# Optimization experiments

Measured on AMD Instinct MI355X. Metric: run time of the kernel, lower is better.

Reference implementation:

```python
import jax, jax.numpy as jnp
import numpy as np

B, T, C, H = 8, 2048, 1024, 64  # batch, context_length, embedding_dim, head_size


def setup_inputs() -> dict:
    key = jax.random.key(0)
    kx, kq, kk, kv = jax.random.split(key, 4)
    s = C ** -0.5  # linear-init-like scale
    return {
        "x": jax.random.normal(kx, (B, T, C), dtype=jnp.float32),
        "Wq": jax.random.normal(kq, (C, H), dtype=jnp.float32) * s,
        "Wk": jax.random.normal(kk, (C, H), dtype=jnp.float32) * s,
        "Wv": jax.random.normal(kv, (C, H), dtype=jnp.float32) * s,
    }


def reference(x, Wq, Wk, Wv):
    Bx, Tx, _ = x.shape
    q = jnp.einsum('btc,ch->bth', x, Wq)
    k = jnp.einsum('btc,ch->bth', x, Wk)
    v = jnp.einsum('btc,ch->bth', x, Wv)
    scale = k.shape[-1] ** -0.5
    scores = jnp.einsum('bth,bsh->bts', q, k) * scale  # [B, T, T]
    causal = jnp.tril(jnp.ones((Tx, Tx), dtype=bool))
    scores = jnp.where(causal, scores, -jnp.inf)
    weights = jax.nn.softmax(scores, axis=-1)
    # dropout is identity in eval mode
    out = jnp.einsum('bts,bsh->bth', weights, v)  # [B, T, H]
    return out
```

## Files before the change

### kernel.cpp

```cpp
#include <hip/hip_runtime.h>
#include <hip/hip_bf16.h>

#define BB 8
#define TT 2048
#define CC 1024
#define HH 64

typedef float f32x4 __attribute__((ext_vector_type(4)));
typedef float f32x16 __attribute__((ext_vector_type(16)));
typedef short s16x8 __attribute__((ext_vector_type(8)));

static __device__ __forceinline__ unsigned short f2bf(float f) {
    unsigned int u = __float_as_uint(f);
    u = (u + 0x7FFFu + ((u >> 16) & 1u)) >> 16;
    return (unsigned short)u;
}

static __device__ __forceinline__ unsigned cvt_pk_bf16(float lo, float hi) {
    unsigned r;
    asm("v_cvt_pk_bf16_f32 %0, %1, %2" : "=v"(r) : "v"(lo), "v"(hi));
    return r;
}

__global__ __launch_bounds__(256) void wt_kernel(
    const float* __restrict__ Wq, const float* __restrict__ Wk,
    const float* __restrict__ Wv, unsigned short* __restrict__ wTf) {
    const int e8 = blockIdx.x * 256 + threadIdx.x;
    const int lane = e8 & 63;
    const int s = (e8 >> 6) & 31;
    const int n16 = e8 >> 11;
    const int sel = n16 >> 2;
    const float* W = (sel == 0) ? Wq : ((sel == 1) ? Wk : Wv);
    const int h = ((n16 & 3) << 4) + (lane & 15);
    const int cb = s * 32 + ((lane >> 4) << 3);
    s16x8 v;
#pragma unroll
    for (int j = 0; j < 8; ++j) v[j] = (short)f2bf(W[(size_t)(cb + j) * HH + h]);
    *reinterpret_cast<s16x8*>(&wTf[(size_t)e8 * 8]) = v;
}

__global__ __launch_bounds__(512, 2) void qkv_kernel(
    const float* __restrict__ x, const unsigned short* __restrict__ wTf,
    unsigned short* __restrict__ Qf, unsigned short* __restrict__ Kf,
    unsigned short* __restrict__ Vf) {
    __shared__ unsigned short xb[2][64 * 128];
    const int tid = threadIdx.x;
    const int wv = tid >> 6, lane = tid & 63;
    const int lo = lane & 15, hi = lane >> 4;
    const int wm = wv >> 2, wn = wv & 3;
    const int rb = blockIdx.x * 64;

    const int srow = tid >> 3, sc = (tid & 7) * 16;
    const float* xsrc = &x[(size_t)(rb + srow) * CC + sc];
    const int swz = (srow & 7) << 3;
    const int wg0 = srow * 128 + (sc ^ swz);
    const int wg1 = srow * 128 + ((sc + 8) ^ swz);

    const int ar0 = (wm * 32 + lo) * 128;
    const int ar1 = ar0 + 16 * 128;
    const int aswz = (lo & 7) << 3;

    f32x4 acc[2][3];
#pragma unroll
    for (int m = 0; m < 2; ++m)
#pragma unroll
        for (int n = 0; n < 3; ++n) acc[m][n] = (f32x4){0.f, 0.f, 0.f, 0.f};

    f32x4 pfA[4], pfB[4];
#pragma unroll
    for (int i = 0; i < 4; ++i) pfA[i] = *reinterpret_cast<const f32x4*>(xsrc + 4 * i);
#pragma unroll
    for (int i = 0; i < 4; ++i) pfB[i] = *reinterpret_cast<const f32x4*>(xsrc + 128 + 4 * i);

    s16x8 bv[4][3];
#define BLOAD(SET, SLOT)                                                       \
    {                                                                          \
        _Pragma("unroll")                                                      \
        for (int n = 0; n < 3; ++n)                                            \
            bv[SET][n] = *reinterpret_cast<const s16x8*>(                      \
                &wTf[(((size_t)(wn * 3 + n) * 32 + (SLOT)) * 64 + lane) * 8]); \
    }
    BLOAD(0, 0)
    BLOAD(1, 1)
    BLOAD(2, 2)

#pragma unroll
    for (int c = 0; c < 8; ++c) {
        unsigned short* wb = xb[c & 1];
        {
            const f32x4* pf = (c & 1) ? pfB : pfA;
            s16x8 w0, w1;
            w0[0] = (short)f2bf(pf[0][0]); w0[1] = (short)f2bf(pf[0][1]);
            w0[2] = (short)f2bf(pf[0][2]); w0[3] = (short)f2bf(pf[0][3]);
            w0[4] = (short)f2bf(pf[1][0]); w0[5] = (short)f2bf(pf[1][1]);
            w0[6] = (short)f2bf(pf[1][2]); w0[7] = (short)f2bf(pf[1][3]);
            w1[0] = (short)f2bf(pf[2][0]); w1[1] = (short)f2bf(pf[2][1]);
            w1[2] = (short)f2bf(pf[2][2]); w1[3] = (short)f2bf(pf[2][3]);
            w1[4] = (short)f2bf(pf[3][0]); w1[5] = (short)f2bf(pf[3][1]);
            w1[6] = (short)f2bf(pf[3][2]); w1[7] = (short)f2bf(pf[3][3]);
            *reinterpret_cast<s16x8*>(&wb[wg0]) = w0;
            *reinterpret_cast<s16x8*>(&wb[wg1]) = w1;
        }
        __syncthreads();
        if (c < 6) {
            if (c & 1) {
#pragma unroll
                for (int i = 0; i < 4; ++i)
                    pfB[i] = *reinterpret_cast<const f32x4*>(xsrc + (c + 2) * 128 + 4 * i);
            } else {
#pragma unroll
                for (int i = 0; i < 4; ++i)
                    pfA[i] = *reinterpret_cast<const f32x4*>(xsrc + (c + 2) * 128 + 4 * i);
            }
        }
        const unsigned short* base = xb[c & 1];
#pragma unroll
        for (int kh = 0; kh < 4; ++kh) {
            const int slot = c * 4 + kh;
            if (slot + 3 < 32) BLOAD((slot + 3) & 3, slot + 3)
            const s16x8 a0 = *reinterpret_cast<const s16x8*>(
                &base[ar0 + ((kh * 32 + hi * 8) ^ aswz)]);
            const s16x8 a1 = *reinterpret_cast<const s16x8*>(
                &base[ar1 + ((kh * 32 + hi * 8) ^ aswz)]);
#pragma unroll
            for (int n = 0; n < 3; ++n) {
                acc[0][n] = __builtin_amdgcn_mfma_f32_16x16x32_bf16(a0, bv[slot & 3][n], acc[0][n], 0, 0, 0);
                acc[1][n] = __builtin_amdgcn_mfma_f32_16x16x32_bf16(a1, bv[slot & 3][n], acc[1][n], 0, 0, 0);
            }
        }
    }
#undef BLOAD

    __syncthreads();
    unsigned short* fr = reinterpret_cast<unsigned short*>(xb);
#pragma unroll
    for (int n = 0; n < 3; ++n) {
        const int n16 = wn * 3 + n;
        const int sel = n16 >> 2;
#pragma unroll
        for (int m = 0; m < 2; ++m) {
#pragma unroll
            for (int r = 0; r < 4; ++r) {
                const int row64 = wm * 32 + m * 16 + 4 * hi + r;
                const int tib = row64 >> 5, tok31 = row64 & 31;
                const int ib = tib * 6144;
                const unsigned short bvv = f2bf(acc[m][n][r]);
                if (sel == 0) {
                    const int s = n16, half = (lo >> 3) & 1, j = lo & 7;
                    fr[ib + (s * 64 + half * 32 + tok31) * 8 + j] = bvv;
                } else if (sel == 1) {
                    const int s = n16 - 4, half = (lo >> 3) & 1, j = lo & 7;
                    fr[ib + 2048 + (s * 64 + half * 32 + tok31) * 8 + j] = bvv;
                } else {
                    const int h = (n16 - 8) * 16 + lo;
                    const int mt = h >> 5;
                    const int s2 = tok31 >> 4, hf = (tok31 >> 3) & 1, jj = tok31 & 7;
                    fr[ib + 4096 + ((mt * 2 + s2) * 64 + hf * 32 + (h & 31)) * 8 + jj] = bvv;
                }
            }
        }
    }
    __syncthreads();
    const int b_ = rb >> 11;
    const int tile0 = (rb & (TT - 1)) >> 5;
#pragma unroll
    for (int i = 0; i < 3; ++i) {
        const int g = tid + 512 * i;
        const int tib = (g >= 768) ? 1 : 0;
        const int rem = g - tib * 768;
        const int buf = rem >> 8;
        const int off = rem & 255;
        const s16x8 val = *reinterpret_cast<const s16x8*>(
            &fr[tib * 6144 + buf * 2048 + off * 8]);
        unsigned short* dst = (buf == 0) ? Qf : ((buf == 1) ? Kf : Vf);
        *reinterpret_cast<s16x8*>(
            &dst[((size_t)b_ * 64 + tile0 + tib) * 2048 + off * 8]) = val;
    }
}

__global__ __launch_bounds__(512, 4) void attn_kernel(
    const unsigned short* __restrict__ Qf, const unsigned short* __restrict__ Kf,
    const unsigned short* __restrict__ Vf, float* __restrict__ out) {
    __shared__ __align__(16) char smem[33792 + 2048];
    float (*OfL)[64][33] = reinterpret_cast<float(*)[64][33]>(smem);
    float (*Mm)[32] = reinterpret_cast<float(*)[32]>(smem + 33792);
    float (*Ml)[32] = reinterpret_cast<float(*)[32]>(smem + 33792 + 1024);

    const int tid = threadIdx.x;
    const int wv = tid >> 6, lane = tid & 63;
    const int q = lane & 31, half = lane >> 5;
    const int b = blockIdx.x & 7;
    const int qt = 63 - (blockIdx.x >> 3);
    const int qbase = qt * 32;
    const float CEXP = 0.125f * 1.44269504f;

    const unsigned short* qp = &Qf[(((size_t)b * 64 + qt) * 256 + lane) * 8];
    s16x8 qf[4];
#pragma unroll
    for (int s = 0; s < 4; ++s) qf[s] = *reinterpret_cast<const s16x8*>(qp + s * 512);

    f32x16 oA, oB;
#pragma unroll
    for (int r = 0; r < 16; ++r) { oA[r] = 0.f; oB[r] = 0.f; }
    float m = -1e30f, l = 0.f;

    for (int t = wv; t <= qt; t += 8) {
        const unsigned short* vp = &Vf[(((size_t)b * 64 + t) * 256 + lane) * 8];
        s16x8 vf[4];
#pragma unroll
        for (int i = 0; i < 4; ++i)
            vf[i] = *reinterpret_cast<const s16x8*>(vp + i * 512);
        const unsigned short* kp = &Kf[(((size_t)b * 64 + t) * 256 + lane) * 8];
        f32x16 sa;
#pragma unroll
        for (int r = 0; r < 16; ++r) sa[r] = 0.f;
#pragma unroll
        for (int s = 0; s < 4; ++s) {
            const s16x8 kf = *reinterpret_cast<const s16x8*>(kp + s * 512);
            sa = __builtin_amdgcn_mfma_f32_32x32x16_bf16(kf, qf[s], sa, 0, 0, 0);
        }
        if (t == qt) {
#pragma unroll
            for (int r = 0; r < 16; ++r) {
                const int key = 4 * half + (r & 3) + 8 * (r >> 2);
                if (key > q) sa[r] = -1e30f;
            }
        }
        float pmax = sa[0];
#pragma unroll
        for (int r = 1; r < 16; ++r) pmax = fmaxf(pmax, sa[r]);
        pmax = fmaxf(pmax, __shfl_xor(pmax, 32));
        if (!__all(pmax <= m + 64.f)) {
            const float mnew = fmaxf(m, pmax);
            const float alpha = exp2f((m - mnew) * CEXP);
            l *= alpha;
#pragma unroll
            for (int r = 0; r < 16; ++r) { oA[r] *= alpha; oB[r] *= alpha; }
            m = mnew;
        }
        float rs = 0.f;
#pragma unroll
        for (int r = 0; r < 16; ++r) {
            const float p = exp2f((sa[r] - m) * CEXP);
            sa[r] = p;
            rs += p;
        }
        l += rs + __shfl_xor(rs, 32);
        unsigned d[8];
#pragma unroll
        for (int i = 0; i < 8; ++i) d[i] = cvt_pk_bf16(sa[2 * i], sa[2 * i + 1]);
        const unsigned snd0 = half ? d[0] : d[2];
        const unsigned snd1 = half ? d[1] : d[3];
        const unsigned snd2 = half ? d[4] : d[6];
        const unsigned snd3 = half ? d[5] : d[7];
        const unsigned rcv0 = __shfl_xor(snd0, 32);
        const unsigned rcv1 = __shfl_xor(snd1, 32);
        const unsigned rcv2 = __shfl_xor(snd2, 32);
        const unsigned rcv3 = __shfl_xor(snd3, 32);
        union { unsigned u[4]; s16x8 v; } f0, f1;
        f0.u[0] = half ? rcv0 : d[0];
        f0.u[1] = half ? rcv1 : d[1];
        f0.u[2] = half ? d[2] : rcv0;
        f0.u[3] = half ? d[3] : rcv1;
        f1.u[0] = half ? rcv2 : d[4];
        f1.u[1] = half ? rcv3 : d[5];
        f1.u[2] = half ? d[6] : rcv2;
        f1.u[3] = half ? d[7] : rcv3;
        oA = __builtin_amdgcn_mfma_f32_32x32x16_bf16(vf[0], f0.v, oA, 0, 0, 0);
        oB = __builtin_amdgcn_mfma_f32_32x32x16_bf16(vf[2], f0.v, oB, 0, 0, 0);
        oA = __builtin_amdgcn_mfma_f32_32x32x16_bf16(vf[1], f1.v, oA, 0, 0, 0);
        oB = __builtin_amdgcn_mfma_f32_32x32x16_bf16(vf[3], f1.v, oB, 0, 0, 0);
    }

#define PUBLISH(slot)                                                      \
    {                                                                      \
        _Pragma("unroll")                                                  \
        for (int r = 0; r < 16; ++r) {                                     \
            const int h0 = (r & 3) + 8 * (r >> 2) + 4 * half;              \
            OfL[slot][h0][q] = oA[r];                                      \
            OfL[slot][h0 + 32][q] = oB[r];                                 \
        }                                                                  \
    }
#define MERGE(slot, srcw)                                                  \
    {                                                                      \
        const float mb = Mm[srcw][q], lb = Ml[srcw][q];                    \
        const float M = fmaxf(m, mb);                                      \
        const float wa = exp2f((m - M) * CEXP);                            \
        const float wb = exp2f((mb - M) * CEXP);                           \
        _Pragma("unroll")                                                  \
        for (int r = 0; r < 16; ++r) {                                     \
            const int h0 = (r & 3) + 8 * (r >> 2) + 4 * half;              \
            oA[r] = oA[r] * wa + OfL[slot][h0][q] * wb;                    \
            oB[r] = oB[r] * wa + OfL[slot][h0 + 32][q] * wb;               \
        }                                                                  \
        l = l * wa + lb * wb;                                              \
        m = M;                                                             \
    }

    if (lane < 32) { Mm[wv][q] = m; Ml[wv][q] = l; }
    if (wv >= 4) PUBLISH(wv - 4);
    __syncthreads();
    if (wv < 4) MERGE(wv, wv + 4);
    __syncthreads();
    if (wv == 2 || wv == 3) {
        PUBLISH(wv - 2);
        if (lane < 32) { Mm[wv][q] = m; Ml[wv][q] = l; }
    }
    __syncthreads();
    if (wv < 2) MERGE(wv, wv + 2);
    __syncthreads();
    if (wv == 1) {
        PUBLISH(1);
        if (lane < 32) { Mm[1][q] = m; Ml[1][q] = l; }
    }
    __syncthreads();
    if (wv == 0) {
        MERGE(1, 1);
        const float inv = 1.f / l;
#pragma unroll
        for (int r = 0; r < 16; ++r) {
            const int h0 = (r & 3) + 8 * (r >> 2) + 4 * half;
            OfL[0][h0][q] = oA[r] * inv;
            OfL[0][h0 + 32][q] = oB[r] * inv;
        }
    }
    __syncthreads();
#pragma unroll
    for (int i = 0; i < 4; ++i) {
        const int idx = tid + 512 * i;
        const int h = idx & 63, q2 = idx >> 6;
        out[((size_t)b * TT + qbase + q2) * HH + h] = OfL[0][h][q2];
    }
#undef PUBLISH
#undef MERGE
}

extern "C" void kernel_launch(void* const* d_in, const int* in_sizes, int n_in,
                              void* d_out, int out_size, void* d_ws, size_t ws_size,
                              hipStream_t stream) {
    (void)in_sizes; (void)n_in; (void)out_size; (void)ws_size;
    const float* x  = (const float*)d_in[0];
    const float* Wq = (const float*)d_in[1];
    const float* Wk = (const float*)d_in[2];
    const float* Wv = (const float*)d_in[3];
    float* out = (float*)d_out;

    char* ws = (char*)d_ws;
    unsigned short* wTf = (unsigned short*)ws;
    unsigned short* Qf  = (unsigned short*)(ws + 393216);
    unsigned short* Kf  = (unsigned short*)(ws + 393216 + 2097152);
    unsigned short* Vf  = (unsigned short*)(ws + 393216 + 4194304);

    wt_kernel<<<96, 256, 0, stream>>>(Wq, Wk, Wv, wTf);
    qkv_kernel<<<256, 512, 0, stream>>>(x, wTf, Qf, Kf, Vf);
    attn_kernel<<<512, 512, 0, stream>>>(Qf, Kf, Vf, out);
}
```

Measured before the change: 42.91 us.

## Stream x into LDS with direct global-to-LDS loads and triple buffering

The QKV projection now copies fp32 x tiles straight from global memory into LDS using global_load_lds, in a three-slot ring, instead of staging them through registers and converting to bf16 before the LDS write. The bf16 conversion moves to the consumer side, where packed cvt instructions run after each LDS read, and each stage covers 64 columns over 16 stages. The aim is to cut register pressure and VALU work in the load path and overlap x fetches with MFMA work. In exchange it uses more LDS (48KB, fp32 tiles) and relies on hand-written waitcnt counts that mix with the weight-fragment global loads, which may serialize more than needed.

```diff
diff --git a/kernel.cpp b/kernel.cpp
--- a/kernel.cpp
+++ b/kernel.cpp
@@ -20,6 +20,12 @@
     unsigned r;
     asm("v_cvt_pk_bf16_f32 %0, %1, %2" : "=v"(r) : "v"(lo), "v"(hi));
     return r;
+}
+
+static __device__ __forceinline__ void gll16(const float* gsrc, void* ldst) {
+    __builtin_amdgcn_global_load_lds(
+        (const __attribute__((address_space(1))) void*)gsrc,
+        (__attribute__((address_space(3))) void*)ldst, 16, 0, 0);
 }
 
 __global__ __launch_bounds__(256) void wt_kernel(
@@ -43,34 +49,24 @@
     const float* __restrict__ x, const unsigned short* __restrict__ wTf,
     unsigned short* __restrict__ Qf, unsigned short* __restrict__ Kf,
     unsigned short* __restrict__ Vf) {
-    __shared__ unsigned short xb[2][64 * 128];
+    __shared__ __align__(16) unsigned char smem[49152];
     const int tid = threadIdx.x;
     const int wv = tid >> 6, lane = tid & 63;
     const int lo = lane & 15, hi = lane >> 4;
     const int wm = wv >> 2, wn = wv & 3;
     const int rb = blockIdx.x * 64;
 
-    const int srow = tid >> 3, sc = (tid & 7) * 16;
-    const float* xsrc = &x[(size_t)(rb + srow) * CC + sc];
-    const int swz = (srow & 7) << 3;
-    const int wg0 = srow * 128 + (sc ^ swz);
-    const int wg1 = srow * 128 + ((sc + 8) ^ swz);
-
-    const int ar0 = (wm * 32 + lo) * 128;
-    const int ar1 = ar0 + 16 * 128;
-    const int aswz = (lo & 7) << 3;
+    const int u0 = 2 * wv, u1 = 2 * wv + 1;
+    const float* src0 = x + ((size_t)(rb + (u0 >> 3) * 32 + ((u0 >> 2) & 1) * 16 + lo)) * CC
+                          + ((u0 >> 1) & 1) * 32 + hi * 8 + (u0 & 1) * 4;
+    const float* src1 = x + ((size_t)(rb + (u1 >> 3) * 32 + ((u1 >> 2) & 1) * 16 + lo)) * CC
+                          + ((u1 >> 1) & 1) * 32 + hi * 8 + (u1 & 1) * 4;
 
     f32x4 acc[2][3];
 #pragma unroll
     for (int m = 0; m < 2; ++m)
 #pragma unroll
         for (int n = 0; n < 3; ++n) acc[m][n] = (f32x4){0.f, 0.f, 0.f, 0.f};
-
-    f32x4 pfA[4], pfB[4];
-#pragma unroll
-    for (int i = 0; i < 4; ++i) pfA[i] = *reinterpret_cast<const f32x4*>(xsrc + 4 * i);
-#pragma unroll
-    for (int i = 0; i < 4; ++i) pfB[i] = *reinterpret_cast<const f32x4*>(xsrc + 128 + 4 * i);
 
     s16x8 bv[4][3];
 #define BLOAD(SET, SLOT)                                                       \
@@ -80,59 +76,58 @@
             bv[SET][n] = *reinterpret_cast<const s16x8*>(                      \
                 &wTf[(((size_t)(wn * 3 + n) * 32 + (SLOT)) * 64 + lane) * 8]); \
     }
-    BLOAD(0, 0)
-    BLOAD(1, 1)
-    BLOAD(2, 2)
-
-#pragma unroll
-    for (int c = 0; c < 8; ++c) {
-        unsigned short* wb = xb[c & 1];
-        {
-            const f32x4* pf = (c & 1) ? pfB : pfA;
-            s16x8 w0, w1;
-            w0[0] = (short)f2bf(pf[0][0]); w0[1] = (short)f2bf(pf[0][1]);
-            w0[2] = (short)f2bf(pf[0][2]); w0[3] = (short)f2bf(pf[0][3]);
-            w0[4] = (short)f2bf(pf[1][0]); w0[5] = (short)f2bf(pf[1][1]);
-            w0[6] = (short)f2bf(pf[1][2]); w0[7] = (short)f2bf(pf[1][3]);
-            w1[0] = (short)f2bf(pf[2][0]); w1[1] = (short)f2bf(pf[2][1]);
-            w1[2] = (short)f2bf(pf[2][2]); w1[3] = (short)f2bf(pf[2][3]);
-            w1[4] = (short)f2bf(pf[3][0]); w1[5] = (short)f2bf(pf[3][1]);
-            w1[6] = (short)f2bf(pf[3][2]); w1[7] = (short)f2bf(pf[3][3]);
-            *reinterpret_cast<s16x8*>(&wb[wg0]) = w0;
-            *reinterpret_cast<s16x8*>(&wb[wg1]) = w1;
-        }
-        __syncthreads();
-        if (c < 6) {
-            if (c & 1) {
-#pragma unroll
-                for (int i = 0; i < 4; ++i)
-                    pfB[i] = *reinterpret_cast<const f32x4*>(xsrc + (c + 2) * 128 + 4 * i);
-            } else {
-#pragma unroll
-                for (int i = 0; i < 4; ++i)
-                    pfA[i] = *reinterpret_cast<const f32x4*>(xsrc + (c + 2) * 128 + 4 * i);
-            }
-        }
-        const unsigned short* base = xb[c & 1];
-#pragma unroll
-        for (int kh = 0; kh < 4; ++kh) {
-            const int slot = c * 4 + kh;
+
+    gll16(src0, smem + u0 * 1024);
+    gll16(src1, smem + u1 * 1024);
+    gll16(src0 + 64, smem + 16384 + u0 * 1024);
+    gll16(src1 + 64, smem + 16384 + u1 * 1024);
+    BLOAD(0, 0) BLOAD(1, 1) BLOAD(2, 2)
+    asm volatile("s_waitcnt vmcnt(2)" ::: "memory");
+    __builtin_amdgcn_s_barrier();
+
+#pragma unroll
+    for (int c = 0; c < 16; ++c) {
+        if (c + 2 < 16) {
+            unsigned char* d = smem + ((c + 2) % 3) * 16384;
+            gll16(src0 + (c + 2) * 64, d + u0 * 1024);
+            gll16(src1 + (c + 2) * 64, d + u1 * 1024);
+        }
+        const unsigned char* base = smem + (c % 3) * 16384;
+#pragma unroll
+        for (int kh = 0; kh < 2; ++kh) {
+            const int slot = 2 * c + kh;
             if (slot + 3 < 32) BLOAD((slot + 3) & 3, slot + 3)
-            const s16x8 a0 = *reinterpret_cast<const s16x8*>(
-                &base[ar0 + ((kh * 32 + hi * 8) ^ aswz)]);
-            const s16x8 a1 = *reinterpret_cast<const s16x8*>(
-                &base[ar1 + ((kh * 32 + hi * 8) ^ aswz)]);
+            union { unsigned u[4]; s16x8 v; } a0, a1;
+            {
+                const int uu = ((wm * 2 + 0) * 2 + kh) * 2;
+                const f32x4 g0 = *reinterpret_cast<const f32x4*>(base + (uu * 64 + lane) * 16);
+                const f32x4 g1 = *reinterpret_cast<const f32x4*>(base + ((uu + 1) * 64 + lane) * 16);
+                a0.u[0] = cvt_pk_bf16(g0[0], g0[1]);
+                a0.u[1] = cvt_pk_bf16(g0[2], g0[3]);
+                a0.u[2] = cvt_pk_bf16(g1[0], g1[1]);
+                a0.u[3] = cvt_pk_bf16(g1[2], g1[3]);
+            }
+            {
+                const int uu = ((wm * 2 + 1) * 2 + kh) * 2;
+                const f32x4 g0 = *reinterpret_cast<const f32x4*>(base + (uu * 64 + lane) * 16);
+                const f32x4 g1 = *reinterpret_cast<const f32x4*>(base + ((uu + 1) * 64 + lane) * 16);
+                a1.u[0] = cvt_pk_bf16(g0[0], g0[1]);
+                a1.u[1] = cvt_pk_bf16(g0[2], g0[3]);
+                a1.u[2] = cvt_pk_bf16(g1[0], g1[1]);
+                a1.u[3] = cvt_pk_bf16(g1[2], g1[3]);
+            }
 #pragma unroll
             for (int n = 0; n < 3; ++n) {
-                acc[0][n] = __builtin_amdgcn_mfma_f32_16x16x32_bf16(a0, bv[slot & 3][n], acc[0][n], 0, 0, 0);
-                acc[1][n] = __builtin_amdgcn_mfma_f32_16x16x32_bf16(a1, bv[slot & 3][n], acc[1][n], 0, 0, 0);
-            }
-        }
+                acc[0][n] = __builtin_amdgcn_mfma_f32_16x16x32_bf16(a0.v, bv[slot & 3][n], acc[0][n], 0, 0, 0);
+                acc[1][n] = __builtin_amdgcn_mfma_f32_16x16x32_bf16(a1.v, bv[slot & 3][n], acc[1][n], 0, 0, 0);
+            }
+        }
+        asm volatile("s_waitcnt vmcnt(4) lgkmcnt(0)" ::: "memory");
+        __builtin_amdgcn_s_barrier();
     }
 #undef BLOAD
 
-    __syncthreads();
-    unsigned short* fr = reinterpret_cast<unsigned short*>(xb);
+    unsigned short* fr = reinterpret_cast<unsigned short*>(smem);
 #pragma unroll
     for (int n = 0; n < 3; ++n) {
         const int n16 = wn * 3 + n;
```

Result: slower. 46.97 us (+9.5%).
